# Kernel tuning notes

Measured on AMD Instinct MI355X. Metric: run time of the kernel, lower is better.

Reference implementation:

```python
import jax, jax.numpy as jnp
import numpy as np

LN_EPS = 1e-5


def setup_inputs() -> dict:
    key = jax.random.key(0)
    ks = jax.random.split(key, 6)
    B, T, D, E, F = 8, 2048, 1024, 8, 4096
    x = jax.random.normal(ks[0], (B, T, D), dtype=jnp.float32)
    router_w = jax.random.normal(ks[1], (E, D), dtype=jnp.float32) * 0.02
    wfc = jax.random.normal(ks[2], (E, F, D), dtype=jnp.float32) * 0.02
    bfc = jnp.zeros((E, F), dtype=jnp.float32)
    wproj = jax.random.normal(ks[3], (E, D, F), dtype=jnp.float32) * 0.02
    bproj = jnp.zeros((E, D), dtype=jnp.float32)
    ln_g = jnp.ones((D,), dtype=jnp.float32)
    ln_b = jnp.zeros((D,), dtype=jnp.float32)
    return {"x": x, "router_w": router_w, "wfc": wfc, "bfc": bfc,
            "wproj": wproj, "bproj": bproj, "ln_g": ln_g, "ln_b": ln_b,
            "top_k": 2}


def reference(x, router_w, wfc, bfc, wproj, bproj, ln_g, ln_b, top_k):
    # Router: [B,T,E] logits, top-k selection, softmax over the k logits.
    router_logits = jnp.einsum('btd,ed->bte', x, router_w)
    top_vals, top_idx = jax.lax.top_k(router_logits, top_k)   # [B,T,K]
    top_probs = jax.nn.softmax(top_vals, axis=-1)             # [B,T,K]

    E = router_w.shape[0]
    out = jnp.zeros_like(x)
    # Dense-per-expert compute with zero gate for unrouted tokens; identical
    # math to the torch gather/scatter loop (dropout inert in eval).
    for e in range(E):
        gate = jnp.sum(jnp.where(top_idx == e, top_probs, 0.0), axis=-1)  # [B,T]
        h = jax.nn.gelu(jnp.einsum('btd,fd->btf', x, wfc[e]) + bfc[e],
                        approximate=False)
        y = jnp.einsum('btf,df->btd', h, wproj[e]) + bproj[e]
        out = out + y * gate[..., None]

    # LayerNorm over hidden dim
    mu = jnp.mean(out, axis=-1, keepdims=True)
    var = jnp.mean(jnp.square(out - mu), axis=-1, keepdims=True)
    out = (out - mu) * jax.lax.rsqrt(var + LN_EPS) * ln_g + ln_b
    return (out, router_logits)
```

## Files before the change

### kernel.cpp

```cpp
#include <hip/hip_runtime.h>

#define NTOK 16384
#define DDIM 1024
#define FDIM 4096
#define NEXP 8
#define PADPAIRS 33792
#define MAXTILES 264
#define TILE2E_PAD 296

#define WS_XB      0ull
#define WS_WFCB    33554432ull
#define WS_WPROJB  100663296ull
#define WS_H       167772160ull

typedef short bf16x8 __attribute__((ext_vector_type(8)));
typedef float f32x4 __attribute__((ext_vector_type(4)));

__device__ __forceinline__ unsigned short f2bf(float f) {
    unsigned int u = __float_as_uint(f);
    u += 0x7fffu + ((u >> 16) & 1u);
    return (unsigned short)(u >> 16);
}

__device__ __forceinline__ void gload16(const unsigned short* g, const unsigned short* lds) {
    __builtin_amdgcn_global_load_lds(
        (const __attribute__((address_space(1))) unsigned int*)(unsigned long long)(const void*)g,
        (__attribute__((address_space(3))) unsigned int*)(unsigned int)(unsigned long long)(const void*)lds,
        16, 0, 0);
}

#define SCHED0() __builtin_amdgcn_sched_barrier(0)

__global__ __launch_bounds__(256) void convert_kernel(const float* __restrict__ src,
                                                      unsigned short* __restrict__ dst) {
    int i = blockIdx.x * 256 + threadIdx.x;
    float4 v = ((const float4*)src)[i];
    ushort4 o;
    o.x = f2bf(v.x); o.y = f2bf(v.y); o.z = f2bf(v.z); o.w = f2bf(v.w);
    ((ushort4*)dst)[i] = o;
}

__global__ __launch_bounds__(256) void router_kernel(const float* __restrict__ x,
                                                     const float* __restrict__ rw,
                                                     unsigned short* __restrict__ xb,
                                                     float* __restrict__ logits,
                                                     int* __restrict__ tok_idx,
                                                     float* __restrict__ tok_gate,
                                                     int* __restrict__ counts) {
    __shared__ float srw[NEXP * DDIM];
    __shared__ int scnt[NEXP];
    int tid = threadIdx.x;
    if (tid < NEXP) scnt[tid] = 0;
    for (int i = tid; i < NEXP * DDIM / 4; i += 256)
        ((float4*)srw)[i] = ((const float4*)rw)[i];
    __syncthreads();

    int wave = tid >> 6, lane = tid & 63;
    const float4* srw4 = (const float4*)srw;

    for (int j = 0; j < 4; j++) {
        int t = blockIdx.x * 16 + wave * 4 + j;
        const float4* xr = (const float4*)(x + (size_t)t * DDIM);
        ushort4* xbr = (ushort4*)(xb + (size_t)t * DDIM);

        float acc[NEXP];
#pragma unroll
        for (int e = 0; e < NEXP; e++) acc[e] = 0.f;

#pragma unroll
        for (int i = 0; i < 4; i++) {
            int k4 = i * 64 + lane;
            float4 xv = xr[k4];
            ushort4 o;
            o.x = f2bf(xv.x); o.y = f2bf(xv.y); o.z = f2bf(xv.z); o.w = f2bf(xv.w);
            xbr[k4] = o;
#pragma unroll
            for (int e = 0; e < NEXP; e++) {
                float4 wv = srw4[e * 256 + k4];
                acc[e] += xv.x * wv.x + xv.y * wv.y + xv.z * wv.z + xv.w * wv.w;
            }
        }
#pragma unroll
        for (int off = 1; off < 64; off <<= 1) {
#pragma unroll
            for (int e = 0; e < NEXP; e++) acc[e] += __shfl_xor(acc[e], off);
        }
        if (lane == 0) {
            float v0 = -1e30f, v1 = -1e30f; int i0 = 0, i1 = 0;
#pragma unroll
            for (int e = 0; e < NEXP; e++) {
                float v = acc[e];
                logits[(size_t)t * NEXP + e] = v;
                if (v > v0)      { v1 = v0; i1 = i0; v0 = v; i0 = e; }
                else if (v > v1) { v1 = v;  i1 = e; }
            }
            float d = __expf(v1 - v0);
            float g0 = 1.f / (1.f + d);
            float g1 = d * g0;
            tok_idx[t * 2 + 0] = i0; tok_idx[t * 2 + 1] = i1;
            tok_gate[t * 2 + 0] = g0; tok_gate[t * 2 + 1] = g1;
            atomicAdd(&scnt[i0], 1);
            atomicAdd(&scnt[i1], 1);
        }
    }
    __syncthreads();
    if (tid < NEXP) atomicAdd(&counts[tid * 16], scnt[tid]);
}

__global__ void seg_plan(const int* __restrict__ counts, int* __restrict__ seg_start,
                         int* __restrict__ tile2e, int* __restrict__ total_tiles,
                         int* __restrict__ pair_token, float* __restrict__ pair_gate) {
    if (threadIdx.x == 0) {
        int cum = 0, tl = 0;
        for (int e = 0; e < NEXP; e++) {
            seg_start[e] = cum;
            int tiles = (counts[e * 16] + 127) >> 7;
            for (int i = 0; i < tiles; i++) tile2e[tl++] = e;
            cum += tiles << 7;
        }
        for (int i = tl; i < TILE2E_PAD; i++) tile2e[i] = -1;
        *total_tiles = tl;
    }
    for (int i = threadIdx.x; i < PADPAIRS; i += 256) {
        pair_token[i] = 0;
        pair_gate[i] = 0.f;
    }
}

__global__ __launch_bounds__(256) void scatter_k(const int* __restrict__ tok_idx,
                                                 const float* __restrict__ tok_gate,
                                                 const int* __restrict__ seg_start,
                                                 int* __restrict__ cursor,
                                                 int* __restrict__ pair_token,
                                                 float* __restrict__ pair_gate) {
    __shared__ int lcnt[NEXP];
    __shared__ int lbase[NEXP];
    int tid = threadIdx.x;
    if (tid < NEXP) lcnt[tid] = 0;
    __syncthreads();
    int t = blockIdx.x * 256 + tid;
    int e0 = tok_idx[t * 2 + 0], e1 = tok_idx[t * 2 + 1];
    float g0 = tok_gate[t * 2 + 0], g1 = tok_gate[t * 2 + 1];
    int r0 = atomicAdd(&lcnt[e0], 1);
    int r1 = atomicAdd(&lcnt[e1], 1);
    __syncthreads();
    if (tid < NEXP) lbase[tid] = atomicAdd(&cursor[tid * 16], lcnt[tid]);
    __syncthreads();
    int p0 = seg_start[e0] + lbase[e0] + r0;
    int p1 = seg_start[e1] + lbase[e1] + r1;
    pair_token[p0] = t; pair_gate[p0] = g0;
    pair_token[p1] = t; pair_gate[p1] = g1;
}

__global__ __launch_bounds__(256, 3) void gemm1_kernel(const unsigned short* __restrict__ xb,
                                                    const unsigned short* __restrict__ wfcb,
                                                    const float* __restrict__ bfc,
                                                    const int* __restrict__ pair_token,
                                                    const int* __restrict__ tile2e,
                                                    int chunk_base,
                                                    unsigned short* __restrict__ h) {
    int tile = chunk_base + blockIdx.y;
    int e = tile2e[tile];
    if (e < 0) return;
    int ftile = blockIdx.x;

    __shared__ unsigned short sA[2][128 * 64];
    __shared__ unsigned short sB[128 * 64];

    int tid = threadIdx.x;
    int wave = tid >> 6, lane = tid & 63;
    int lrow = lane >> 3;
    int kblk = (lane & 7) ^ lrow;

    const unsigned short* wB = wfcb + (size_t)e * FDIM * DDIM + (size_t)ftile * 128 * DDIM;
    const unsigned short* aBase[4];
    const unsigned short* bBase[4];
#pragma unroll
    for (int t = 0; t < 4; t++) {
        int row = wave * 32 + t * 8 + lrow;
        aBase[t] = xb + (size_t)pair_token[tile * 128 + row] * DDIM + kblk * 8;
        bBase[t] = wB + (size_t)row * DDIM + kblk * 8;
    }

    f32x4 zero = {0.f, 0.f, 0.f, 0.f};
    f32x4 acc[4][4];
#pragma unroll
    for (int i = 0; i < 4; i++)
#pragma unroll
        for (int j = 0; j < 4; j++) acc[i][j] = zero;

    int wm = (wave >> 1) * 64, wn = (wave & 1) * 64;
    int quad = lane >> 4, l16 = lane & 15;
    int r7 = l16 & 7;

    constexpr int NK = DDIM / 64;
#pragma unroll
    for (int t = 0; t < 4; t++) {
        gload16(aBase[t], &sA[0][(wave * 32 + t * 8) * 64]);
        aBase[t] += 64;
    }
    SCHED0();

#pragma unroll 1
    for (int k = 0; k < NK - 1; ++k) {
#pragma unroll
        for (int t = 0; t < 4; t++) {
            gload16(bBase[t], &sB[(wave * 32 + t * 8) * 64]);
            bBase[t] += 64;
        }
        const unsigned short* sAn = sA[(k + 1) & 1];
#pragma unroll
        for (int t = 0; t < 4; t++) {
            gload16(aBase[t], &sAn[(wave * 32 + t * 8) * 64]);
            aBase[t] += 64;
        }
        SCHED0();
        asm volatile("s_waitcnt vmcnt(4)" ::: "memory");
        SCHED0();
        __builtin_amdgcn_s_barrier();
        SCHED0();
        const unsigned short* sAc = sA[k & 1];
#pragma unroll
        for (int ks = 0; ks < 64; ks += 32) {
            int g = (ks >> 3) + quad;
            bf16x8 af[4], bfr[4];
#pragma unroll
            for (int i = 0; i < 4; i++) {
                int row = wm + i * 16 + l16;
                af[i] = *(const bf16x8*)&sAc[row * 64 + ((g ^ r7) << 3)];
            }
#pragma unroll
            for (int j = 0; j < 4; j++) {
                int row = wn + j * 16 + l16;
                bfr[j] = *(const bf16x8*)&sB[row * 64 + ((g ^ r7) << 3)];
            }
#pragma unroll
            for (int i = 0; i < 4; i++)
#pragma unroll
                for (int j = 0; j < 4; j++)
                    acc[i][j] = __builtin_amdgcn_mfma_f32_16x16x32_bf16(af[i], bfr[j], acc[i][j], 0, 0, 0);
        }
        SCHED0();
        __builtin_amdgcn_s_barrier();
        SCHED0();
    }
    {
#pragma unroll
        for (int t = 0; t < 4; t++)
            gload16(bBase[t], &sB[(wave * 32 + t * 8) * 64]);
        SCHED0();
        asm volatile("s_waitcnt vmcnt(0)" ::: "memory");
        SCHED0();
        __builtin_amdgcn_s_barrier();
        SCHED0();
        const unsigned short* sAc = sA[(NK - 1) & 1];
#pragma unroll
        for (int ks = 0; ks < 64; ks += 32) {
            int g = (ks >> 3) + quad;
            bf16x8 af[4], bfr[4];
#pragma unroll
            for (int i = 0; i < 4; i++) {
                int row = wm + i * 16 + l16;
                af[i] = *(const bf16x8*)&sAc[row * 64 + ((g ^ r7) << 3)];
            }
#pragma unroll
            for (int j = 0; j < 4; j++) {
                int row = wn + j * 16 + l16;
                bfr[j] = *(const bf16x8*)&sB[row * 64 + ((g ^ r7) << 3)];
            }
#pragma unroll
            for (int i = 0; i < 4; i++)
#pragma unroll
                for (int j = 0; j < 4; j++)
                    acc[i][j] = __builtin_amdgcn_mfma_f32_16x16x32_bf16(af[i], bfr[j], acc[i][j], 0, 0, 0);
        }
    }

    unsigned short* hrow_base = h + (size_t)blockIdx.y * 128 * FDIM;
#pragma unroll
    for (int i = 0; i < 4; i++) {
#pragma unroll
        for (int j = 0; j < 4; j++) {
            int col = wn + j * 16 + l16;
            int f = ftile * 128 + col;
            float bias = bfc[e * FDIM + f];
#pragma unroll
            for (int r = 0; r < 4; r++) {
                int row = wm + i * 16 + quad * 4 + r;
                float v = acc[i][j][r] + bias;
                v = 0.5f * v * (1.f + erff(v * 0.70710678118654752f));
                hrow_base[(size_t)row * FDIM + f] = f2bf(v);
            }
        }
    }
}

__global__ __launch_bounds__(256, 3) void gemm2_kernel(const unsigned short* __restrict__ h,
                                                    const unsigned short* __restrict__ wprojb,
                                                    const float* __restrict__ bproj,
                                                    const int* __restrict__ pair_token,
                                                    const float* __restrict__ pair_gate,
                                                    const int* __restrict__ tile2e,
                                                    int chunk_base,
                                                    float* __restrict__ out) {
    int flat = blockIdx.x + (blockIdx.y << 3);
    int xcd  = flat & 7;
    int slot = flat >> 3;
    int tl   = ((slot >> 3) << 3) + xcd;
    int dtile = slot & 7;

    int tile = chunk_base + tl;
    int e = tile2e[tile];
    if (e < 0) return;

    __shared__ unsigned short sA[2][128 * 64];
    __shared__ unsigned short sB[128 * 64];

    int tid = threadIdx.x;
    int wave = tid >> 6, lane = tid & 63;
    int lrow = lane >> 3;
    int kblk = (lane & 7) ^ lrow;

    const unsigned short* hA = h + (size_t)tl * 128 * FDIM;
    const unsigned short* wB = wprojb + (size_t)e * DDIM * FDIM + (size_t)dtile * 128 * FDIM;
    const unsigned short* aBase[4];
    const unsigned short* bBase[4];
#pragma unroll
    for (int t = 0; t < 4; t++) {
        int row = wave * 32 + t * 8 + lrow;
        aBase[t] = hA + (size_t)row * FDIM + kblk * 8;
        bBase[t] = wB + (size_t)row * FDIM + kblk * 8;
    }

    f32x4 zero = {0.f, 0.f, 0.f, 0.f};
    f32x4 acc[4][4];
#pragma unroll
    for (int i = 0; i < 4; i++)
#pragma unroll
        for (int j = 0; j < 4; j++) acc[i][j] = zero;

    int wm = (wave >> 1) * 64, wn = (wave & 1) * 64;
    int quad = lane >> 4, l16 = lane & 15;
    int r7 = l16 & 7;

    constexpr int NK = FDIM / 64;
#pragma unroll
    for (int t = 0; t < 4; t++) {
        gload16(aBase[t], &sA[0][(wave * 32 + t * 8) * 64]);
        aBase[t] += 64;
    }
    SCHED0();

#pragma unroll 1
    for (int k = 0; k < NK - 1; ++k) {
#pragma unroll
        for (int t = 0; t < 4; t++) {
            gload16(bBase[t], &sB[(wave * 32 + t * 8) * 64]);
            bBase[t] += 64;
        }
        const unsigned short* sAn = sA[(k + 1) & 1];
#pragma unroll
        for (int t = 0; t < 4; t++) {
            gload16(aBase[t], &sAn[(wave * 32 + t * 8) * 64]);
            aBase[t] += 64;
        }
        SCHED0();
        asm volatile("s_waitcnt vmcnt(4)" ::: "memory");
        SCHED0();
        __builtin_amdgcn_s_barrier();
        SCHED0();
        const unsigned short* sAc = sA[k & 1];
#pragma unroll
        for (int ks = 0; ks < 64; ks += 32) {
            int g = (ks >> 3) + quad;
            bf16x8 af[4], bfr[4];
#pragma unroll
            for (int i = 0; i < 4; i++) {
                int row = wm + i * 16 + l16;
                af[i] = *(const bf16x8*)&sAc[row * 64 + ((g ^ r7) << 3)];
            }
#pragma unroll
            for (int j = 0; j < 4; j++) {
                int row = wn + j * 16 + l16;
                bfr[j] = *(const bf16x8*)&sB[row * 64 + ((g ^ r7) << 3)];
            }
#pragma unroll
            for (int i = 0; i < 4; i++)
#pragma unroll
                for (int j = 0; j < 4; j++)
                    acc[i][j] = __builtin_amdgcn_mfma_f32_16x16x32_bf16(af[i], bfr[j], acc[i][j], 0, 0, 0);
        }
        SCHED0();
        __builtin_amdgcn_s_barrier();
        SCHED0();
    }
    {
#pragma unroll
        for (int t = 0; t < 4; t++)
            gload16(bBase[t], &sB[(wave * 32 + t * 8) * 64]);
        SCHED0();
        asm volatile("s_waitcnt vmcnt(0)" ::: "memory");
        SCHED0();
        __builtin_amdgcn_s_barrier();
        SCHED0();
        const unsigned short* sAc = sA[(NK - 1) & 1];
#pragma unroll
        for (int ks = 0; ks < 64; ks += 32) {
            int g = (ks >> 3) + quad;
            bf16x8 af[4], bfr[4];
#pragma unroll
            for (int i = 0; i < 4; i++) {
                int row = wm + i * 16 + l16;
                af[i] = *(const bf16x8*)&sAc[row * 64 + ((g ^ r7) << 3)];
            }
#pragma unroll
            for (int j = 0; j < 4; j++) {
                int row = wn + j * 16 + l16;
                bfr[j] = *(const bf16x8*)&sB[row * 64 + ((g ^ r7) << 3)];
            }
#pragma unroll
            for (int i = 0; i < 4; i++)
#pragma unroll
                for (int j = 0; j < 4; j++)
                    acc[i][j] = __builtin_amdgcn_mfma_f32_16x16x32_bf16(af[i], bfr[j], acc[i][j], 0, 0, 0);
        }
    }

#pragma unroll
    for (int i = 0; i < 4; i++) {
#pragma unroll
        for (int j = 0; j < 4; j++) {
            int col = wn + j * 16 + l16;
            int d = dtile * 128 + col;
            float bias = bproj[e * DDIM + d];
#pragma unroll
            for (int r = 0; r < 4; r++) {
                int row = wm + i * 16 + quad * 4 + r;
                int tok = pair_token[tile * 128 + row];
                float gate = pair_gate[tile * 128 + row];
                float v = (acc[i][j][r] + bias) * gate;
                atomicAdd(&out[(size_t)tok * DDIM + d], v);
            }
        }
    }
}

__global__ __launch_bounds__(256) void ln_kernel(float* __restrict__ out,
                                                 const float* __restrict__ g,
                                                 const float* __restrict__ b) {
    __shared__ float s1[4], s2[4];
    int t = blockIdx.x, tid = threadIdx.x;
    float* row = out + (size_t)t * DDIM;
    float4 v = ((const float4*)row)[tid];
    float sum = v.x + v.y + v.z + v.w;
    float sq = v.x * v.x + v.y * v.y + v.z * v.z + v.w * v.w;
#pragma unroll
    for (int off = 32; off > 0; off >>= 1) {
        sum += __shfl_down(sum, off);
        sq  += __shfl_down(sq, off);
    }
    int wave = tid >> 6, lane = tid & 63;
    if (lane == 0) { s1[wave] = sum; s2[wave] = sq; }
    __syncthreads();
    float tot = s1[0] + s1[1] + s1[2] + s1[3];
    float totsq = s2[0] + s2[1] + s2[2] + s2[3];
    float mu = tot * (1.f / DDIM);
    float var = totsq * (1.f / DDIM) - mu * mu;
    float rs = rsqrtf(var + 1e-5f);
    float4 gv = ((const float4*)g)[tid];
    float4 bv = ((const float4*)b)[tid];
    float4 o;
    o.x = (v.x - mu) * rs * gv.x + bv.x;
    o.y = (v.y - mu) * rs * gv.y + bv.y;
    o.z = (v.z - mu) * rs * gv.z + bv.z;
    o.w = (v.w - mu) * rs * gv.w + bv.w;
    ((float4*)row)[tid] = o;
}

extern "C" void kernel_launch(void* const* d_in, const int* in_sizes, int n_in,
                              void* d_out, int out_size, void* d_ws, size_t ws_size,
                              hipStream_t stream) {
    const float* x   = (const float*)d_in[0];
    const float* rw  = (const float*)d_in[1];
    const float* wfc = (const float*)d_in[2];
    const float* bfc = (const float*)d_in[3];
    const float* wpr = (const float*)d_in[4];
    const float* bpr = (const float*)d_in[5];
    const float* lng = (const float*)d_in[6];
    const float* lnb = (const float*)d_in[7];

    float* out = (float*)d_out;
    float* logits = out + (size_t)NTOK * DDIM;

    char* ws = (char*)d_ws;
    unsigned short* xb     = (unsigned short*)(ws + WS_XB);
    unsigned short* wfcb   = (unsigned short*)(ws + WS_WFCB);
    unsigned short* wprojb = (unsigned short*)(ws + WS_WPROJB);
    unsigned short* hbuf   = (unsigned short*)(ws + WS_H);

    size_t aux_bytes = (size_t)PADPAIRS * 8 + (size_t)NTOK * 16 + 16384;
    int ct = 72;
    if (ws_size >= WS_H + (size_t)136 * 128 * FDIM * 2 + aux_bytes) ct = 136;
    int nchunks = (MAXTILES + ct - 1) / ct;

    char* aux = ws + WS_H + (size_t)ct * 128 * FDIM * 2;
    int*   ptok  = (int*)aux;
    float* pgate = (float*)(aux + (size_t)PADPAIRS * 4);
    int*   tidx  = (int*)(aux + (size_t)PADPAIRS * 8);
    float* tgate = (float*)(aux + (size_t)PADPAIRS * 8 + (size_t)NTOK * 8);
    int*   meta  = (int*)(aux + (size_t)PADPAIRS * 8 + (size_t)NTOK * 16);
    int* counts = meta;
    int* cursor = meta + 128;
    int* segs   = meta + 256;
    int* total  = meta + 264;
    int* tile2e = meta + 272;

    hipMemsetAsync(out, 0, (size_t)NTOK * DDIM * sizeof(float), stream);
    hipMemsetAsync(meta, 0, 4096, stream);

    convert_kernel<<<(NEXP * FDIM * DDIM) / 4 / 256, 256, 0, stream>>>(wfc, wfcb);
    convert_kernel<<<(NEXP * DDIM * FDIM) / 4 / 256, 256, 0, stream>>>(wpr, wprojb);
    router_kernel<<<NTOK / 16, 256, 0, stream>>>(x, rw, xb, logits, tidx, tgate, counts);
    seg_plan<<<1, 256, 0, stream>>>(counts, segs, tile2e, total, ptok, pgate);
    scatter_k<<<NTOK / 256, 256, 0, stream>>>(tidx, tgate, segs, cursor, ptok, pgate);

    for (int c = 0; c < nchunks; c++) {
        gemm1_kernel<<<dim3(FDIM / 128, ct), 256, 0, stream>>>(
            xb, wfcb, bfc, ptok, tile2e, c * ct, hbuf);
        gemm2_kernel<<<dim3(8, ct), 256, 0, stream>>>(
            hbuf, wprojb, bpr, ptok, pgate, tile2e, c * ct, out);
    }
    ln_kernel<<<NTOK, 256, 0, stream>>>(out, lng, lnb);
}
```

Before: 1.184 ms.

## Double-buffer B tiles, replace atomic scatter with per-pair output buffer, single chunk

Both grouped GEMMs now double-buffer the weight (B) tile in LDS alongside A, with one wait and one barrier per k-step, and drop occupancy hints from 3 to 2 blocks per CU. When the workspace is large enough, gemm2 writes gated per-pair rows to a dense ypair buffer instead of doing atomicAdd into out. The LayerNorm kernel then sums each token's two pair rows through a new tok2pos map, which also removes the zero-memset of out. The h buffer is sized for all 264 tiles so only one chunk launches. This costs a large extra workspace (about 138MB for ypair) and more LDS per block, and whether mode 2 runs depends on the workspace size.

```diff
diff --git a/kernel.cpp b/kernel.cpp
--- a/kernel.cpp
+++ b/kernel.cpp
@@ -132,7 +132,8 @@
                                                  const int* __restrict__ seg_start,
                                                  int* __restrict__ cursor,
                                                  int* __restrict__ pair_token,
-                                                 float* __restrict__ pair_gate) {
+                                                 float* __restrict__ pair_gate,
+                                                 int* __restrict__ tok2pos) {
     __shared__ int lcnt[NEXP];
     __shared__ int lbase[NEXP];
     int tid = threadIdx.x;
@@ -150,9 +151,11 @@
     int p1 = seg_start[e1] + lbase[e1] + r1;
     pair_token[p0] = t; pair_gate[p0] = g0;
     pair_token[p1] = t; pair_gate[p1] = g1;
-}
-
-__global__ __launch_bounds__(256, 3) void gemm1_kernel(const unsigned short* __restrict__ xb,
+    tok2pos[t * 2 + 0] = p0;
+    tok2pos[t * 2 + 1] = p1;
+}
+
+__global__ __launch_bounds__(256, 2) void gemm1_kernel(const unsigned short* __restrict__ xb,
                                                     const unsigned short* __restrict__ wfcb,
                                                     const float* __restrict__ bfc,
                                                     const int* __restrict__ pair_token,
@@ -165,7 +168,7 @@
     int ftile = blockIdx.x;
 
     __shared__ unsigned short sA[2][128 * 64];
-    __shared__ unsigned short sB[128 * 64];
+    __shared__ unsigned short sB[2][128 * 64];
 
     int tid = threadIdx.x;
     int wave = tid >> 6, lane = tid & 63;
@@ -197,29 +200,28 @@
 #pragma unroll
     for (int t = 0; t < 4; t++) {
         gload16(aBase[t], &sA[0][(wave * 32 + t * 8) * 64]);
-        aBase[t] += 64;
-    }
+        gload16(bBase[t], &sB[0][(wave * 32 + t * 8) * 64]);
+        aBase[t] += 64; bBase[t] += 64;
+    }
+    SCHED0();
+    asm volatile("s_waitcnt vmcnt(0)" ::: "memory");
+    SCHED0();
+    __builtin_amdgcn_s_barrier();
     SCHED0();
 
 #pragma unroll 1
     for (int k = 0; k < NK - 1; ++k) {
-#pragma unroll
-        for (int t = 0; t < 4; t++) {
-            gload16(bBase[t], &sB[(wave * 32 + t * 8) * 64]);
-            bBase[t] += 64;
-        }
         const unsigned short* sAn = sA[(k + 1) & 1];
+        const unsigned short* sBn = sB[(k + 1) & 1];
 #pragma unroll
         for (int t = 0; t < 4; t++) {
             gload16(aBase[t], &sAn[(wave * 32 + t * 8) * 64]);
-            aBase[t] += 64;
-        }
-        SCHED0();
-        asm volatile("s_waitcnt vmcnt(4)" ::: "memory");
-        SCHED0();
-        __builtin_amdgcn_s_barrier();
+            gload16(bBase[t], &sBn[(wave * 32 + t * 8) * 64]);
+            aBase[t] += 64; bBase[t] += 64;
+        }
         SCHED0();
         const unsigned short* sAc = sA[k & 1];
+        const unsigned short* sBc = sB[k & 1];
 #pragma unroll
         for (int ks = 0; ks < 64; ks += 32) {
             int g = (ks >> 3) + quad;
@@ -232,7 +234,7 @@
 #pragma unroll
             for (int j = 0; j < 4; j++) {
                 int row = wn + j * 16 + l16;
-                bfr[j] = *(const bf16x8*)&sB[row * 64 + ((g ^ r7) << 3)];
+                bfr[j] = *(const bf16x8*)&sBc[row * 64 + ((g ^ r7) << 3)];
             }
 #pragma unroll
             for (int i = 0; i < 4; i++)
@@ -241,19 +243,14 @@
                     acc[i][j] = __builtin_amdgcn_mfma_f32_16x16x32_bf16(af[i], bfr[j], acc[i][j], 0, 0, 0);
         }
         SCHED0();
+        asm volatile("s_waitcnt vmcnt(0)" ::: "memory");
+        SCHED0();
         __builtin_amdgcn_s_barrier();
         SCHED0();
     }
     {
-#pragma unroll
-        for (int t = 0; t < 4; t++)
-            gload16(bBase[t], &sB[(wave * 32 + t * 8) * 64]);
-        SCHED0();
-        asm volatile("s_waitcnt vmcnt(0)" ::: "memory");
-        SCHED0();
-        __builtin_amdgcn_s_barrier();
-        SCHED0();
         const unsigned short* sAc = sA[(NK - 1) & 1];
+        const unsigned short* sBc = sB[(NK - 1) & 1];
 #pragma unroll
         for (int ks = 0; ks < 64; ks += 32) {
             int g = (ks >> 3) + quad;
@@ -266,7 +263,7 @@
 #pragma unroll
             for (int j = 0; j < 4; j++) {
                 int row = wn + j * 16 + l16;
-                bfr[j] = *(const bf16x8*)&sB[row * 64 + ((g ^ r7) << 3)];
+                bfr[j] = *(const bf16x8*)&sBc[row * 64 + ((g ^ r7) << 3)];
             }
 #pragma unroll
             for (int i = 0; i < 4; i++)
@@ -295,14 +292,16 @@
     }
 }
 
-__global__ __launch_bounds__(256, 3) void gemm2_kernel(const unsigned short* __restrict__ h,
+__global__ __launch_bounds__(256, 2) void gemm2_kernel(const unsigned short* __restrict__ h,
                                                     const unsigned short* __restrict__ wprojb,
                                                     const float* __restrict__ bproj,
                                                     const int* __restrict__ pair_token,
                                                     const float* __restrict__ pair_gate,
                                                     const int* __restrict__ tile2e,
                                                     int chunk_base,
-                                                    float* __restrict__ out) {
+                                                    float* __restrict__ out,
+                                                    float* __restrict__ ypair,
+                                                    int use_ypair) {
     int flat = blockIdx.x + (blockIdx.y << 3);
     int xcd  = flat & 7;
     int slot = flat >> 3;
@@ -314,7 +313,7 @@
     if (e < 0) return;
 
     __shared__ unsigned short sA[2][128 * 64];
-    __shared__ unsigned short sB[128 * 64];
+    __shared__ unsigned short sB[2][128 * 64];
 
     int tid = threadIdx.x;
     int wave = tid >> 6, lane = tid & 63;
@@ -347,29 +346,28 @@
 #pragma unroll
     for (int t = 0; t < 4; t++) {
         gload16(aBase[t], &sA[0][(wave * 32 + t * 8) * 64]);
-        aBase[t] += 64;
-    }
+        gload16(bBase[t], &sB[0][(wave * 32 + t * 8) * 64]);
+        aBase[t] += 64; bBase[t] += 64;
+    }
+    SCHED0();
+    asm volatile("s_waitcnt vmcnt(0)" ::: "memory");
+    SCHED0();
+    __builtin_amdgcn_s_barrier();
     SCHED0();
 
 #pragma unroll 1
     for (int k = 0; k < NK - 1; ++k) {
-#pragma unroll
-        for (int t = 0; t < 4; t++) {
-            gload16(bBase[t], &sB[(wave * 32 + t * 8) * 64]);
-            bBase[t] += 64;
-        }
         const unsigned short* sAn = sA[(k + 1) & 1];
+        const unsigned short* sBn = sB[(k + 1) & 1];
 #pragma unroll
         for (int t = 0; t < 4; t++) {
             gload16(aBase[t], &sAn[(wave * 32 + t * 8) * 64]);
-            aBase[t] += 64;
-        }
-        SCHED0();
-        asm volatile("s_waitcnt vmcnt(4)" ::: "memory");
-        SCHED0();
-        __builtin_amdgcn_s_barrier();
+            gload16(bBase[t], &sBn[(wave * 32 + t * 8) * 64]);
+            aBase[t] += 64; bBase[t] += 64;
+        }
         SCHED0();
         const unsigned short* sAc = sA[k & 1];
+        const unsigned short* sBc = sB[k & 1];
 #pragma unroll
         for (int ks = 0; ks < 64; ks += 32) {
             int g = (ks >> 3) + quad;
@@ -382,7 +380,7 @@
 #pragma unroll
             for (int j = 0; j < 4; j++) {
                 int row = wn + j * 16 + l16;
-                bfr[j] = *(const bf16x8*)&sB[row * 64 + ((g ^ r7) << 3)];
+                bfr[j] = *(const bf16x8*)&sBc[row * 64 + ((g ^ r7) << 3)];
             }
 #pragma unroll
             for (int i = 0; i < 4; i++)
@@ -391,19 +389,14 @@
                     acc[i][j] = __builtin_amdgcn_mfma_f32_16x16x32_bf16(af[i], bfr[j], acc[i][j], 0, 0, 0);
         }
         SCHED0();
+        asm volatile("s_waitcnt vmcnt(0)" ::: "memory");
+        SCHED0();
         __builtin_amdgcn_s_barrier();
         SCHED0();
     }
     {
-#pragma unroll
-        for (int t = 0; t < 4; t++)
-            gload16(bBase[t], &sB[(wave * 32 + t * 8) * 64]);
-        SCHED0();
-        asm volatile("s_waitcnt vmcnt(0)" ::: "memory");
-        SCHED0();
-        __builtin_amdgcn_s_barrier();
-        SCHED0();
         const unsigned short* sAc = sA[(NK - 1) & 1];
+        const unsigned short* sBc = sB[(NK - 1) & 1];
 #pragma unroll
         for (int ks = 0; ks < 64; ks += 32) {
             int g = (ks >> 3) + quad;
@@ -416,7 +409,7 @@
 #pragma unroll
             for (int j = 0; j < 4; j++) {
                 int row = wn + j * 16 + l16;
-                bfr[j] = *(const bf16x8*)&sB[row * 64 + ((g ^ r7) << 3)];
+                bfr[j] = *(const bf16x8*)&sBc[row * 64 + ((g ^ r7) << 3)];
             }
 #pragma unroll
             for (int i = 0; i < 4; i++)
@@ -426,32 +419,61 @@
         }
     }
 
-#pragma unroll
-    for (int i = 0; i < 4; i++) {
-#pragma unroll
-        for (int j = 0; j < 4; j++) {
-            int col = wn + j * 16 + l16;
-            int d = dtile * 128 + col;
-            float bias = bproj[e * DDIM + d];
-#pragma unroll
-            for (int r = 0; r < 4; r++) {
-                int row = wm + i * 16 + quad * 4 + r;
-                int tok = pair_token[tile * 128 + row];
-                float gate = pair_gate[tile * 128 + row];
-                float v = (acc[i][j][r] + bias) * gate;
-                atomicAdd(&out[(size_t)tok * DDIM + d], v);
+    if (use_ypair) {
+        float* yb = ypair + (size_t)(tile * 128) * DDIM + dtile * 128;
+#pragma unroll
+        for (int i = 0; i < 4; i++) {
+#pragma unroll
+            for (int j = 0; j < 4; j++) {
+                int col = wn + j * 16 + l16;
+                float bias = bproj[e * DDIM + dtile * 128 + col];
+#pragma unroll
+                for (int r = 0; r < 4; r++) {
+                    int row = wm + i * 16 + quad * 4 + r;
+                    float gate = pair_gate[tile * 128 + row];
+                    yb[(size_t)row * DDIM + col] = (acc[i][j][r] + bias) * gate;
+                }
+            }
+        }
+    } else {
+#pragma unroll
+        for (int i = 0; i < 4; i++) {
+#pragma unroll
+            for (int j = 0; j < 4; j++) {
+                int col = wn + j * 16 + l16;
+                int d = dtile * 128 + col;
+                float bias = bproj[e * DDIM + d];
+#pragma unroll
+                for (int r = 0; r < 4; r++) {
+                    int row = wm + i * 16 + quad * 4 + r;
+                    int tok = pair_token[tile * 128 + row];
+                    float gate = pair_gate[tile * 128 + row];
+                    float v = (acc[i][j][r] + bias) * gate;
+                    atomicAdd(&out[(size_t)tok * DDIM + d], v);
+                }
             }
         }
     }
 }
 
 __global__ __launch_bounds__(256) void ln_kernel(float* __restrict__ out,
+                                                 const float* __restrict__ ypair,
+                                                 const int* __restrict__ tok2pos,
+                                                 int use_ypair,
                                                  const float* __restrict__ g,
                                                  const float* __restrict__ b) {
     __shared__ float s1[4], s2[4];
     int t = blockIdx.x, tid = threadIdx.x;
     float* row = out + (size_t)t * DDIM;
-    float4 v = ((const float4*)row)[tid];
+    float4 v;
+    if (use_ypair) {
+        int p0 = tok2pos[t * 2 + 0], p1 = tok2pos[t * 2 + 1];
+        float4 a = ((const float4*)(ypair + (size_t)p0 * DDIM))[tid];
+        float4 c = ((const float4*)(ypair + (size_t)p1 * DDIM))[tid];
+        v.x = a.x + c.x; v.y = a.y + c.y; v.z = a.z + c.z; v.w = a.w + c.w;
+    } else {
+        v = ((const float4*)row)[tid];
+    }
     float sum = v.x + v.y + v.z + v.w;
     float sq = v.x * v.x + v.y * v.y + v.z * v.z + v.w * v.w;
 #pragma unroll
@@ -498,37 +520,47 @@
     unsigned short* wprojb = (unsigned short*)(ws + WS_WPROJB);
     unsigned short* hbuf   = (unsigned short*)(ws + WS_H);
 
-    size_t aux_bytes = (size_t)PADPAIRS * 8 + (size_t)NTOK * 16 + 16384;
-    int ct = 72;
-    if (ws_size >= WS_H + (size_t)136 * 128 * FDIM * 2 + aux_bytes) ct = 136;
+    const size_t YPAIR_BYTES = (size_t)PADPAIRS * DDIM * 4;
+    size_t aux_bytes = (size_t)PADPAIRS * 8 + (size_t)NTOK * 24 + 16384;
+    size_t h264 = (size_t)264 * 128 * FDIM * 2;
+    size_t h72  = (size_t)72 * 128 * FDIM * 2;
+    int mode, ct;
+    if (ws_size >= WS_H + h264 + YPAIR_BYTES + aux_bytes)      { mode = 2; ct = 264; }
+    else if (ws_size >= WS_H + h264 + aux_bytes)               { mode = 1; ct = 264; }
+    else                                                       { mode = 0; ct = 72; }
     int nchunks = (MAXTILES + ct - 1) / ct;
-
-    char* aux = ws + WS_H + (size_t)ct * 128 * FDIM * 2;
+    size_t h_bytes = (size_t)ct * 128 * FDIM * 2;
+
+    char* ypair_base = ws + WS_H + h_bytes;
+    float* ypair = (float*)ypair_base;
+    char* aux = ypair_base + (mode == 2 ? YPAIR_BYTES : 0);
     int*   ptok  = (int*)aux;
     float* pgate = (float*)(aux + (size_t)PADPAIRS * 4);
     int*   tidx  = (int*)(aux + (size_t)PADPAIRS * 8);
     float* tgate = (float*)(aux + (size_t)PADPAIRS * 8 + (size_t)NTOK * 8);
-    int*   meta  = (int*)(aux + (size_t)PADPAIRS * 8 + (size_t)NTOK * 16);
+    int*   t2p   = (int*)(aux + (size_t)PADPAIRS * 8 + (size_t)NTOK * 16);
+    int*   meta  = (int*)(aux + (size_t)PADPAIRS * 8 + (size_t)NTOK * 24);
     int* counts = meta;
     int* cursor = meta + 128;
     int* segs   = meta + 256;
     int* total  = meta + 264;
     int* tile2e = meta + 272;
 
-    hipMemsetAsync(out, 0, (size_t)NTOK * DDIM * sizeof(float), stream);
+    if (mode != 2)
+        hipMemsetAsync(out, 0, (size_t)NTOK * DDIM * sizeof(float), stream);
     hipMemsetAsync(meta, 0, 4096, stream);
 
     convert_kernel<<<(NEXP * FDIM * DDIM) / 4 / 256, 256, 0, stream>>>(wfc, wfcb);
     convert_kernel<<<(NEXP * DDIM * FDIM) / 4 / 256, 256, 0, stream>>>(wpr, wprojb);
     router_kernel<<<NTOK / 16, 256, 0, stream>>>(x, rw, xb, logits, tidx, tgate, counts);
     seg_plan<<<1, 256, 0, stream>>>(counts, segs, tile2e, total, ptok, pgate);
-    scatter_k<<<NTOK / 256, 256, 0, stream>>>(tidx, tgate, segs, cursor, ptok, pgate);
+    scatter_k<<<NTOK / 256, 256, 0, stream>>>(tidx, tgate, segs, cursor, ptok, pgate, t2p);
 
     for (int c = 0; c < nchunks; c++) {
         gemm1_kernel<<<dim3(FDIM / 128, ct), 256, 0, stream>>>(
             xb, wfcb, bfc, ptok, tile2e, c * ct, hbuf);
         gemm2_kernel<<<dim3(8, ct), 256, 0, stream>>>(
-            hbuf, wprojb, bpr, ptok, pgate, tile2e, c * ct, out);
-    }
-    ln_kernel<<<NTOK, 256, 0, stream>>>(out, lng, lnb);
-}
+            hbuf, wprojb, bpr, ptok, pgate, tile2e, c * ct, out, ypair, mode == 2 ? 1 : 0);
+    }
+    ln_kernel<<<NTOK, 256, 0, stream>>>(out, ypair, t2p, mode == 2 ? 1 : 0, lng, lnb);
+}
```

After: 1.282 ms. 1.08x slower.
